# Performance work log

Measured on AMD Instinct MI355X. Metric: run time of the kernel, lower is better.

Reference implementation:

```python
import jax, jax.numpy as jnp
import numpy as np

HID = 128   # hidden_dim
NCLS = 10   # n_classes
B = 64      # number of graphs in the batched heterograph
NC, NP, NN = 100000, 400000, 150000  # component / port / net node counts
E = 400000  # edges per edge type


def setup_inputs() -> dict:
    key = jax.random.key(0)
    ks = jax.random.split(key, 32)
    f32 = jnp.float32

    def w(k, shape, fan_in):
        return jax.random.normal(k, shape, dtype=f32) * (1.0 / np.sqrt(fan_in))

    inp = {
        "h_comp": jax.random.normal(ks[0], (NC, 1), f32),
        "h_port": jax.random.normal(ks[1], (NP, 2), f32),
        "h_net": jax.random.normal(ks[2], (NN, 1), f32),
        "e_cp_src": jax.random.randint(ks[3], (E,), 0, NC, dtype=jnp.int32),
        "e_cp_dst": jax.random.randint(ks[4], (E,), 0, NP, dtype=jnp.int32),
        "e_pn_src": jax.random.randint(ks[5], (E,), 0, NP, dtype=jnp.int32),
        "e_pn_dst": jax.random.randint(ks[6], (E,), 0, NN, dtype=jnp.int32),
        "gid_comp": jnp.sort(jax.random.randint(ks[7], (NC,), 0, B, dtype=jnp.int32)),
        "gid_port": jnp.sort(jax.random.randint(ks[8], (NP,), 0, B, dtype=jnp.int32)),
        "gid_net": jnp.sort(jax.random.randint(ks[9], (NN,), 0, B, dtype=jnp.int32)),
        # GraphConv weights/biases per (layer, edge_type)
        "W1_cp": w(ks[10], (1, HID), 1), "b1_cp": jnp.zeros((HID,), f32),
        "W1_pn": w(ks[11], (2, HID), 2), "b1_pn": jnp.zeros((HID,), f32),
        "W2_cp": w(ks[12], (HID, HID), HID), "b2_cp": jnp.zeros((HID,), f32),
        "W2_pn": w(ks[13], (HID, HID), HID), "b2_pn": jnp.zeros((HID,), f32),
        "W3_cp": w(ks[14], (HID, HID), HID), "b3_cp": jnp.zeros((HID,), f32),
        "W3_pn": w(ks[15], (HID, HID), HID), "b3_pn": jnp.zeros((HID,), f32),
        # classify MLP (input dim 4 = 1+2+1 pooled original features)
        "Wc1": w(ks[16], (4, HID), 4), "bc1": jnp.zeros((HID,), f32),
        "Wc2": w(ks[17], (HID, HID), HID), "bc2": jnp.zeros((HID,), f32),
        "Wc3": w(ks[18], (HID, NCLS), HID), "bc3": jnp.zeros((NCLS,), f32),
    }
    return inp


def reference(h_comp, h_port, h_net,
              e_cp_src, e_cp_dst, e_pn_src, e_pn_dst,
              gid_comp, gid_port, gid_net,
              W1_cp, b1_cp, W1_pn, b1_pn,
              W2_cp, b2_cp, W2_pn, b2_pn,
              W3_cp, b3_cp, W3_pn, b3_pn,
              Wc1, bc1, Wc2, bc2, Wc3, bc3):
    seg = jax.ops.segment_sum

    # --- HeteroGraphConv layers (faithful to original forward, including its
    # bug: DGL HeteroGraphConv drops node types with no incoming relation, so
    # 'component' vanishes after conv1 and 'port' after conv2; conv3 runs on an
    # empty dict; conv outputs are never written back to g, hence dead code).
    # GraphConv(norm='none'): dst = sum_{edges} (x_src @ W) + b
    port1 = jax.nn.relu(seg((h_comp @ W1_cp)[e_cp_src], e_cp_dst, num_segments=NP) + b1_cp)
    net1 = jax.nn.relu(seg((h_port @ W1_pn)[e_pn_src], e_pn_dst, num_segments=NN) + b1_pn)
    net2 = jax.nn.relu(seg((port1 @ W2_pn)[e_pn_src], e_pn_dst, num_segments=NN) + b2_pn)
    # conv3: skipped entirely (no src types remain in the feature dict)
    del net1, net2  # never used by the original module's output path

    # --- dgl.mean_nodes reads g.nodes[*].data['h'] = ORIGINAL input features
    def gmean(x, gid):
        s = seg(x, gid, num_segments=B)
        c = seg(jnp.ones((x.shape[0], 1), x.dtype), gid, num_segments=B)
        return s / jnp.maximum(c, 1.0)

    hg = jnp.concatenate([gmean(h_comp, gid_comp),
                          gmean(h_port, gid_port),
                          gmean(h_net, gid_net)], axis=1)  # [B, 4]

    h = jax.nn.relu(hg @ Wc1 + bc1)
    h = jax.nn.relu(h @ Wc2 + bc2)
    return h @ Wc3 + bc3  # [B, n_classes]
```

## Files before the change

kernel.cpp:

```cpp
#include <hip/hip_runtime.h>
#include <hip/hip_bf16.h>


#define NGRAPH 64
#define NB_COMP 120
#define NB_PORT 723
#define NB_NET  181
#define NSLOT (NB_COMP + NB_PORT + NB_NET)


template <int NF>
__device__ void reduce_type(const float* __restrict__ h, const int* __restrict__ gid, int n,
                            float (*bins)[NGRAPH][4],
                            int nblocks, int bid) {
    int nv = (n + 3) >> 2;
    int per = (nv + nblocks - 1) / nblocks;
    int start = bid * per;
    int end = min(nv, start + per);
    int set = threadIdx.x & 3;

    int first = start * 4;
    int last = min(end * 4, n) - 1;
    if (first > last) return;

    int g_lo = gid[first];
    int g_hi = gid[last];

    if (g_lo == g_hi) {
        float s0 = 0.f, s1 = 0.f, cnt = 0.f;
        for (int iv = start + (int)threadIdx.x; iv < end; iv += (int)blockDim.x) {
            int i = iv * 4;
            if (i + 3 < n) {
                if (NF == 1) {
                    float4 hv = ((const float4*)h)[iv];
                    s0 += (hv.x + hv.y) + (hv.z + hv.w);
                } else {
                    float4 ha = ((const float4*)h)[iv * 2];
                    float4 hb = ((const float4*)h)[iv * 2 + 1];
                    s0 += ha.x + ha.z + hb.x + hb.z;
                    s1 += ha.y + ha.w + hb.y + hb.w;
                }
                cnt += 4.f;
            } else {
                for (int t = 0; t < 4 && i + t < n; ++t) {
                    if (NF == 1) { s0 += h[i + t]; }
                    else { s0 += h[(i + t) * 2]; s1 += h[(i + t) * 2 + 1]; }
                    cnt += 1.f;
                }
            }
        }
#pragma unroll
        for (int off = 32; off > 0; off >>= 1) {
            s0 += __shfl_down(s0, off);
            if (NF == 2) s1 += __shfl_down(s1, off);
            cnt += __shfl_down(cnt, off);
        }
        if ((threadIdx.x & 63) == 0) {
            int wset = threadIdx.x >> 6;
            atomicAdd(&bins[wset][g_lo][0], s0);
            if (NF == 2) atomicAdd(&bins[wset][g_lo][1], s1);
            atomicAdd(&bins[wset][g_lo][2], cnt);
        }
        return;
    }

    int cur = -1;
    float s0 = 0.f, s1 = 0.f, cnt = 0.f;

    for (int iv = start + (int)threadIdx.x; iv < end; iv += (int)blockDim.x) {
        int i = iv * 4;
        int g[4];
        float v0[4], v1[4];
        if (i + 3 < n) {
            int4 g4 = ((const int4*)gid)[iv];
            g[0] = g4.x; g[1] = g4.y; g[2] = g4.z; g[3] = g4.w;
            if (NF == 1) {
                float4 hv = ((const float4*)h)[iv];
                v0[0] = hv.x; v0[1] = hv.y; v0[2] = hv.z; v0[3] = hv.w;
            } else {
                float4 ha = ((const float4*)h)[iv * 2];
                float4 hb = ((const float4*)h)[iv * 2 + 1];
                v0[0] = ha.x; v1[0] = ha.y; v0[1] = ha.z; v1[1] = ha.w;
                v0[2] = hb.x; v1[2] = hb.y; v0[3] = hb.z; v1[3] = hb.w;
            }
        } else {
#pragma unroll
            for (int t = 0; t < 4; ++t) {
                if (i + t < n) {
                    g[t] = gid[i + t];
                    if (NF == 1) { v0[t] = h[i + t]; }
                    else { v0[t] = h[(i + t) * 2]; v1[t] = h[(i + t) * 2 + 1]; }
                } else {
                    g[t] = -2;
                    v0[t] = 0.f; v1[t] = 0.f;
                }
            }
        }
#pragma unroll
        for (int t = 0; t < 4; ++t) {
            if (g[t] == -2) continue;
            if (g[t] != cur) {
                if (cur >= 0) {
                    atomicAdd(&bins[set][cur][0], s0);
                    if (NF == 2) atomicAdd(&bins[set][cur][1], s1);
                    atomicAdd(&bins[set][cur][2], cnt);
                }
                cur = g[t]; s0 = 0.f; s1 = 0.f; cnt = 0.f;
            }
            s0 += v0[t];
            if (NF == 2) s1 += v1[t];
            cnt += 1.f;
        }
    }
    if (cur >= 0) {
        atomicAdd(&bins[set][cur][0], s0);
        if (NF == 2) atomicAdd(&bins[set][cur][1], s1);
        atomicAdd(&bins[set][cur][2], cnt);
    }
}

__global__ __launch_bounds__(256) void reduce_kernel(
    const float* __restrict__ h_comp, const float* __restrict__ h_port,
    const float* __restrict__ h_net,
    const int* __restrict__ gid_comp, const int* __restrict__ gid_port,
    const int* __restrict__ gid_net,
    int n_comp, int n_port, int n_net,
    float4* __restrict__ ws4) {
    __shared__ float bins[4][NGRAPH][4];
    int tid = threadIdx.x;
    int bid = blockIdx.x;

    for (int i = tid; i < 4 * NGRAPH * 4; i += 256) ((float*)bins)[i] = 0.f;
    __syncthreads();

    if (bid < NB_COMP) {
        reduce_type<1>(h_comp, gid_comp, n_comp, bins, NB_COMP, bid);
    } else if (bid < NB_COMP + NB_PORT) {
        reduce_type<2>(h_port, gid_port, n_port, bins, NB_PORT, bid - NB_COMP);
    } else {
        reduce_type<1>(h_net, gid_net, n_net, bins, NB_NET, bid - NB_COMP - NB_PORT);
    }
    __syncthreads();

    if (tid < NGRAPH) {
        float s0 = bins[0][tid][0] + bins[1][tid][0] + bins[2][tid][0] + bins[3][tid][0];
        float s1 = bins[0][tid][1] + bins[1][tid][1] + bins[2][tid][1] + bins[3][tid][1];
        float c  = bins[0][tid][2] + bins[1][tid][2] + bins[2][tid][2] + bins[3][tid][2];
        ws4[(size_t)tid * NSLOT + bid] = make_float4(s0, s1, c, 0.f);
    }
}

__global__ __launch_bounds__(256) void mlp_kernel(
    const float4* __restrict__ ws4,
    const float* __restrict__ Wc1, const float* __restrict__ bc1,
    const float* __restrict__ Wc2, const float* __restrict__ bc2,
    const float* __restrict__ Wc3, const float* __restrict__ bc3,
    float* __restrict__ out) {
    __shared__ float wred[4][8];
    __shared__ float hgs[4];
    __shared__ float h1[128];
    __shared__ float part[2][128];
    __shared__ float h2[128];
    __shared__ float l3[16][12];

    int g = blockIdx.x;
    int tid = threadIdx.x;

    float cs = 0.f, cc = 0.f, p0 = 0.f, p1 = 0.f, pc = 0.f, ns = 0.f, nc = 0.f;
    for (int s = tid; s < NSLOT; s += 256) {
        float4 v = ws4[(size_t)g * NSLOT + s];
        if (s < NB_COMP) { cs += v.x; cc += v.z; }
        else if (s < NB_COMP + NB_PORT) { p0 += v.x; p1 += v.y; pc += v.z; }
        else { ns += v.x; nc += v.z; }
    }
#pragma unroll
    for (int off = 32; off > 0; off >>= 1) {
        cs += __shfl_down(cs, off); cc += __shfl_down(cc, off);
        p0 += __shfl_down(p0, off); p1 += __shfl_down(p1, off);
        pc += __shfl_down(pc, off); ns += __shfl_down(ns, off);
        nc += __shfl_down(nc, off);
    }
    int wave = tid >> 6;
    if ((tid & 63) == 0) {
        wred[wave][0] = cs; wred[wave][1] = cc; wred[wave][2] = p0; wred[wave][3] = p1;
        wred[wave][4] = pc; wred[wave][5] = ns; wred[wave][6] = nc;
    }
    __syncthreads();
    if (tid == 0) {
        float t0 = wred[0][0] + wred[1][0] + wred[2][0] + wred[3][0];
        float t1 = wred[0][1] + wred[1][1] + wred[2][1] + wred[3][1];
        float t2 = wred[0][2] + wred[1][2] + wred[2][2] + wred[3][2];
        float t3 = wred[0][3] + wred[1][3] + wred[2][3] + wred[3][3];
        float t4 = wred[0][4] + wred[1][4] + wred[2][4] + wred[3][4];
        float t5 = wred[0][5] + wred[1][5] + wred[2][5] + wred[3][5];
        float t6 = wred[0][6] + wred[1][6] + wred[2][6] + wred[3][6];
        hgs[0] = t0 / fmaxf(t1, 1.f);
        hgs[1] = t2 / fmaxf(t4, 1.f);
        hgs[2] = t3 / fmaxf(t4, 1.f);
        hgs[3] = t5 / fmaxf(t6, 1.f);
    }
    __syncthreads();

    if (tid < 128) {
        float v = hgs[0] * Wc1[tid] + hgs[1] * Wc1[128 + tid] +
                  hgs[2] * Wc1[256 + tid] + hgs[3] * Wc1[384 + tid] + bc1[tid];
        h1[tid] = fmaxf(v, 0.f);
    }
    __syncthreads();

    {
        int j = tid & 127;
        int h = tid >> 7;
        float acc = 0.f;
#pragma unroll
        for (int kk = 0; kk < 64; kk += 4) {
            int k = h * 64 + kk;
            float4 hh = *(const float4*)&h1[k];
            acc += hh.x * Wc2[(k + 0) * 128 + j] + hh.y * Wc2[(k + 1) * 128 + j] +
                   hh.z * Wc2[(k + 2) * 128 + j] + hh.w * Wc2[(k + 3) * 128 + j];
        }
        part[h][j] = acc;
    }
    __syncthreads();
    if (tid < 128) h2[tid] = fmaxf(part[0][tid] + part[1][tid] + bc2[tid], 0.f);
    __syncthreads();

    if (tid < 160) {
        int c = tid % 10;
        int seg = tid / 10;
        float a = 0.f;
#pragma unroll
        for (int k = seg * 8; k < seg * 8 + 8; ++k) a += h2[k] * Wc3[k * 10 + c];
        l3[seg][c] = a;
    }
    __syncthreads();
    if (tid < 10) {
        float a = bc3[tid];
#pragma unroll
        for (int s = 0; s < 16; ++s) a += l3[s][tid];
        out[g * 10 + tid] = a;
    }
}

extern "C" void kernel_launch(void* const* d_in, const int* in_sizes, int n_in,
                              void* d_out, int out_size, void* d_ws, size_t ws_size,
                              hipStream_t stream) {
    const float* h_comp = (const float*)d_in[0];
    const float* h_port = (const float*)d_in[1];
    const float* h_net  = (const float*)d_in[2];
    const int* gid_comp = (const int*)d_in[7];
    const int* gid_port = (const int*)d_in[8];
    const int* gid_net  = (const int*)d_in[9];
    const float* Wc1 = (const float*)d_in[22];
    const float* bc1 = (const float*)d_in[23];
    const float* Wc2 = (const float*)d_in[24];
    const float* bc2 = (const float*)d_in[25];
    const float* Wc3 = (const float*)d_in[26];
    const float* bc3 = (const float*)d_in[27];

    int n_comp = in_sizes[0];
    int n_port = in_sizes[1] / 2;
    int n_net  = in_sizes[2];

    float4* ws4 = (float4*)d_ws;
    float* out = (float*)d_out;

    reduce_kernel<<<NSLOT, 256, 0, stream>>>(
        h_comp, h_port, h_net, gid_comp, gid_port, gid_net,
        n_comp, n_port, n_net, ws4);

    mlp_kernel<<<NGRAPH, 256, 0, stream>>>(ws4, Wc1, bc1, Wc2, bc2, Wc3, bc3, out);
}
```

Measured before the change: 119.3 us.

## Fuse segment-mean and MLP into one per-graph kernel using binary-searched ranges

Replaces the two-kernel design (1024-block atomic binning plus per-graph MLP) with a single kernel of 64 blocks, one per graph. Each block finds its contiguous node ranges in the sorted gid arrays through a wave-parallel 64-ary search, then sums the features directly with float4 loads and derives counts from the range lengths. This removes a kernel launch, the workspace round trip and the atomics. The cost is that only 64 blocks of 512 threads stream about 2.6 MB, which may underuse the GPU's memory bandwidth.

```diff
diff --git a/kernel.cpp b/kernel.cpp
--- a/kernel.cpp
+++ b/kernel.cpp
@@ -1,203 +1,132 @@
 #include <hip/hip_runtime.h>
-#include <hip/hip_bf16.h>
 
 
 #define NGRAPH 64
-#define NB_COMP 120
-#define NB_PORT 723
-#define NB_NET  181
-#define NSLOT (NB_COMP + NB_PORT + NB_NET)
-
-
-template <int NF>
-__device__ void reduce_type(const float* __restrict__ h, const int* __restrict__ gid, int n,
-                            float (*bins)[NGRAPH][4],
-                            int nblocks, int bid) {
-    int nv = (n + 3) >> 2;
-    int per = (nv + nblocks - 1) / nblocks;
-    int start = bid * per;
-    int end = min(nv, start + per);
-    int set = threadIdx.x & 3;
-
-    int first = start * 4;
-    int last = min(end * 4, n) - 1;
-    if (first > last) return;
-
-    int g_lo = gid[first];
-    int g_hi = gid[last];
-
-    if (g_lo == g_hi) {
-        float s0 = 0.f, s1 = 0.f, cnt = 0.f;
-        for (int iv = start + (int)threadIdx.x; iv < end; iv += (int)blockDim.x) {
-            int i = iv * 4;
-            if (i + 3 < n) {
-                if (NF == 1) {
-                    float4 hv = ((const float4*)h)[iv];
-                    s0 += (hv.x + hv.y) + (hv.z + hv.w);
-                } else {
-                    float4 ha = ((const float4*)h)[iv * 2];
-                    float4 hb = ((const float4*)h)[iv * 2 + 1];
-                    s0 += ha.x + ha.z + hb.x + hb.z;
-                    s1 += ha.y + ha.w + hb.y + hb.w;
-                }
-                cnt += 4.f;
-            } else {
-                for (int t = 0; t < 4 && i + t < n; ++t) {
-                    if (NF == 1) { s0 += h[i + t]; }
-                    else { s0 += h[(i + t) * 2]; s1 += h[(i + t) * 2 + 1]; }
-                    cnt += 1.f;
-                }
-            }
-        }
-#pragma unroll
-        for (int off = 32; off > 0; off >>= 1) {
-            s0 += __shfl_down(s0, off);
-            if (NF == 2) s1 += __shfl_down(s1, off);
-            cnt += __shfl_down(cnt, off);
-        }
-        if ((threadIdx.x & 63) == 0) {
-            int wset = threadIdx.x >> 6;
-            atomicAdd(&bins[wset][g_lo][0], s0);
-            if (NF == 2) atomicAdd(&bins[wset][g_lo][1], s1);
-            atomicAdd(&bins[wset][g_lo][2], cnt);
-        }
-        return;
-    }
-
-    int cur = -1;
-    float s0 = 0.f, s1 = 0.f, cnt = 0.f;
-
-    for (int iv = start + (int)threadIdx.x; iv < end; iv += (int)blockDim.x) {
-        int i = iv * 4;
-        int g[4];
-        float v0[4], v1[4];
-        if (i + 3 < n) {
-            int4 g4 = ((const int4*)gid)[iv];
-            g[0] = g4.x; g[1] = g4.y; g[2] = g4.z; g[3] = g4.w;
-            if (NF == 1) {
-                float4 hv = ((const float4*)h)[iv];
-                v0[0] = hv.x; v0[1] = hv.y; v0[2] = hv.z; v0[3] = hv.w;
-            } else {
-                float4 ha = ((const float4*)h)[iv * 2];
-                float4 hb = ((const float4*)h)[iv * 2 + 1];
-                v0[0] = ha.x; v1[0] = ha.y; v0[1] = ha.z; v1[1] = ha.w;
-                v0[2] = hb.x; v1[2] = hb.y; v0[3] = hb.z; v1[3] = hb.w;
-            }
+#define BLK 512
+
+__device__ __forceinline__ int wave_lb(const int* __restrict__ a, int n, int key) {
+    int lane = threadIdx.x & 63;
+    int lo = 0;
+    int len = n;
+    while (len > 0) {
+        int chunk = (len + 63) >> 6;
+        int off = lane * chunk;
+        bool valid = off < len;
+        int v = valid ? a[lo + off] : 0;
+        unsigned long long m = __ballot(valid && (v < key));
+        int c = __popcll(m);
+        if (c == 0) {
+            len = 0;
         } else {
-#pragma unroll
-            for (int t = 0; t < 4; ++t) {
-                if (i + t < n) {
-                    g[t] = gid[i + t];
-                    if (NF == 1) { v0[t] = h[i + t]; }
-                    else { v0[t] = h[(i + t) * 2]; v1[t] = h[(i + t) * 2 + 1]; }
-                } else {
-                    g[t] = -2;
-                    v0[t] = 0.f; v1[t] = 0.f;
-                }
-            }
-        }
-#pragma unroll
-        for (int t = 0; t < 4; ++t) {
-            if (g[t] == -2) continue;
-            if (g[t] != cur) {
-                if (cur >= 0) {
-                    atomicAdd(&bins[set][cur][0], s0);
-                    if (NF == 2) atomicAdd(&bins[set][cur][1], s1);
-                    atomicAdd(&bins[set][cur][2], cnt);
-                }
-                cur = g[t]; s0 = 0.f; s1 = 0.f; cnt = 0.f;
-            }
-            s0 += v0[t];
-            if (NF == 2) s1 += v1[t];
-            cnt += 1.f;
-        }
-    }
-    if (cur >= 0) {
-        atomicAdd(&bins[set][cur][0], s0);
-        if (NF == 2) atomicAdd(&bins[set][cur][1], s1);
-        atomicAdd(&bins[set][cur][2], cnt);
-    }
+            int nlo = lo + (c - 1) * chunk + 1;
+            int hi = lo + min(c * chunk, len);
+            lo = nlo;
+            len = hi - nlo;
+        }
+    }
+    return lo;
 }
 
-__global__ __launch_bounds__(256) void reduce_kernel(
+__global__ __launch_bounds__(BLK) void fused_kernel(
     const float* __restrict__ h_comp, const float* __restrict__ h_port,
     const float* __restrict__ h_net,
     const int* __restrict__ gid_comp, const int* __restrict__ gid_port,
     const int* __restrict__ gid_net,
     int n_comp, int n_port, int n_net,
-    float4* __restrict__ ws4) {
-    __shared__ float bins[4][NGRAPH][4];
-    int tid = threadIdx.x;
-    int bid = blockIdx.x;
-
-    for (int i = tid; i < 4 * NGRAPH * 4; i += 256) ((float*)bins)[i] = 0.f;
-    __syncthreads();
-
-    if (bid < NB_COMP) {
-        reduce_type<1>(h_comp, gid_comp, n_comp, bins, NB_COMP, bid);
-    } else if (bid < NB_COMP + NB_PORT) {
-        reduce_type<2>(h_port, gid_port, n_port, bins, NB_PORT, bid - NB_COMP);
-    } else {
-        reduce_type<1>(h_net, gid_net, n_net, bins, NB_NET, bid - NB_COMP - NB_PORT);
-    }
-    __syncthreads();
-
-    if (tid < NGRAPH) {
-        float s0 = bins[0][tid][0] + bins[1][tid][0] + bins[2][tid][0] + bins[3][tid][0];
-        float s1 = bins[0][tid][1] + bins[1][tid][1] + bins[2][tid][1] + bins[3][tid][1];
-        float c  = bins[0][tid][2] + bins[1][tid][2] + bins[2][tid][2] + bins[3][tid][2];
-        ws4[(size_t)tid * NSLOT + bid] = make_float4(s0, s1, c, 0.f);
-    }
-}
-
-__global__ __launch_bounds__(256) void mlp_kernel(
-    const float4* __restrict__ ws4,
     const float* __restrict__ Wc1, const float* __restrict__ bc1,
     const float* __restrict__ Wc2, const float* __restrict__ bc2,
     const float* __restrict__ Wc3, const float* __restrict__ bc3,
     float* __restrict__ out) {
-    __shared__ float wred[4][8];
+    __shared__ int rng[6];
+    __shared__ float wred[BLK / 64][4];
     __shared__ float hgs[4];
     __shared__ float h1[128];
-    __shared__ float part[2][128];
+    __shared__ float part[4][128];
     __shared__ float h2[128];
     __shared__ float l3[16][12];
 
-    int g = blockIdx.x;
-    int tid = threadIdx.x;
-
-    float cs = 0.f, cc = 0.f, p0 = 0.f, p1 = 0.f, pc = 0.f, ns = 0.f, nc = 0.f;
-    for (int s = tid; s < NSLOT; s += 256) {
-        float4 v = ws4[(size_t)g * NSLOT + s];
-        if (s < NB_COMP) { cs += v.x; cc += v.z; }
-        else if (s < NB_COMP + NB_PORT) { p0 += v.x; p1 += v.y; pc += v.z; }
-        else { ns += v.x; nc += v.z; }
-    }
+    const int g = blockIdx.x;
+    const int tid = threadIdx.x;
+    const int wave = tid >> 6;
+
+    if (wave == 0) {
+        int lo = wave_lb(gid_comp, n_comp, g);
+        int hi = wave_lb(gid_comp, n_comp, g + 1);
+        if ((tid & 63) == 0) { rng[0] = lo; rng[1] = hi; }
+    } else if (wave == 1) {
+        int lo = wave_lb(gid_port, n_port, g);
+        int hi = wave_lb(gid_port, n_port, g + 1);
+        if ((tid & 63) == 0) { rng[2] = lo; rng[3] = hi; }
+    } else if (wave == 2) {
+        int lo = wave_lb(gid_net, n_net, g);
+        int hi = wave_lb(gid_net, n_net, g + 1);
+        if ((tid & 63) == 0) { rng[4] = lo; rng[5] = hi; }
+    }
+    __syncthreads();
+
+    const int c0 = rng[0], c1 = rng[1];
+    const int p0 = rng[2], p1 = rng[3];
+    const int q0 = rng[4], q1 = rng[5];
+
+    float sc = 0.f, s0 = 0.f, s1 = 0.f, sn = 0.f;
+
+    {
+        int a4 = min(c1, (c0 + 3) & ~3);
+        for (int i = c0 + tid; i < a4; i += BLK) sc += h_comp[i];
+        int nv = (c1 - a4) >> 2;
+        const float4* hv = (const float4*)(h_comp + a4);
+        for (int iv = tid; iv < nv; iv += BLK) {
+            float4 v = hv[iv];
+            sc += (v.x + v.y) + (v.z + v.w);
+        }
+        for (int i = a4 + nv * 4 + tid; i < c1; i += BLK) sc += h_comp[i];
+    }
+    {
+        int a2 = min(p1, (p0 + 1) & ~1);
+        for (int i = p0 + tid; i < a2; i += BLK) { s0 += h_port[2 * i]; s1 += h_port[2 * i + 1]; }
+        int nv = (p1 - a2) >> 1;
+        const float4* hv = (const float4*)(h_port + 2 * a2);
+        for (int iv = tid; iv < nv; iv += BLK) {
+            float4 v = hv[iv];
+            s0 += v.x + v.z;
+            s1 += v.y + v.w;
+        }
+        for (int i = a2 + nv * 2 + tid; i < p1; i += BLK) { s0 += h_port[2 * i]; s1 += h_port[2 * i + 1]; }
+    }
+    {
+        int a4 = min(q1, (q0 + 3) & ~3);
+        for (int i = q0 + tid; i < a4; i += BLK) sn += h_net[i];
+        int nv = (q1 - a4) >> 2;
+        const float4* hv = (const float4*)(h_net + a4);
+        for (int iv = tid; iv < nv; iv += BLK) {
+            float4 v = hv[iv];
+            sn += (v.x + v.y) + (v.z + v.w);
+        }
+        for (int i = a4 + nv * 4 + tid; i < q1; i += BLK) sn += h_net[i];
+    }
+
 #pragma unroll
     for (int off = 32; off > 0; off >>= 1) {
-        cs += __shfl_down(cs, off); cc += __shfl_down(cc, off);
-        p0 += __shfl_down(p0, off); p1 += __shfl_down(p1, off);
-        pc += __shfl_down(pc, off); ns += __shfl_down(ns, off);
-        nc += __shfl_down(nc, off);
-    }
-    int wave = tid >> 6;
+        sc += __shfl_down(sc, off);
+        s0 += __shfl_down(s0, off);
+        s1 += __shfl_down(s1, off);
+        sn += __shfl_down(sn, off);
+    }
     if ((tid & 63) == 0) {
-        wred[wave][0] = cs; wred[wave][1] = cc; wred[wave][2] = p0; wred[wave][3] = p1;
-        wred[wave][4] = pc; wred[wave][5] = ns; wred[wave][6] = nc;
+        wred[wave][0] = sc; wred[wave][1] = s0;
+        wred[wave][2] = s1; wred[wave][3] = sn;
     }
     __syncthreads();
     if (tid == 0) {
-        float t0 = wred[0][0] + wred[1][0] + wred[2][0] + wred[3][0];
-        float t1 = wred[0][1] + wred[1][1] + wred[2][1] + wred[3][1];
-        float t2 = wred[0][2] + wred[1][2] + wred[2][2] + wred[3][2];
-        float t3 = wred[0][3] + wred[1][3] + wred[2][3] + wred[3][3];
-        float t4 = wred[0][4] + wred[1][4] + wred[2][4] + wred[3][4];
-        float t5 = wred[0][5] + wred[1][5] + wred[2][5] + wred[3][5];
-        float t6 = wred[0][6] + wred[1][6] + wred[2][6] + wred[3][6];
-        hgs[0] = t0 / fmaxf(t1, 1.f);
-        hgs[1] = t2 / fmaxf(t4, 1.f);
-        hgs[2] = t3 / fmaxf(t4, 1.f);
-        hgs[3] = t5 / fmaxf(t6, 1.f);
+        float a = 0.f, b = 0.f, c = 0.f, d = 0.f;
+#pragma unroll
+        for (int w = 0; w < BLK / 64; ++w) {
+            a += wred[w][0]; b += wred[w][1]; c += wred[w][2]; d += wred[w][3];
+        }
+        hgs[0] = a / fmaxf((float)(c1 - c0), 1.f);
+        hgs[1] = b / fmaxf((float)(p1 - p0), 1.f);
+        hgs[2] = c / fmaxf((float)(p1 - p0), 1.f);
+        hgs[3] = d / fmaxf((float)(q1 - q0), 1.f);
     }
     __syncthreads();
 
@@ -210,19 +139,20 @@
 
     {
         int j = tid & 127;
-        int h = tid >> 7;
+        int hq = tid >> 7;
         float acc = 0.f;
 #pragma unroll
-        for (int kk = 0; kk < 64; kk += 4) {
-            int k = h * 64 + kk;
+        for (int kk = 0; kk < 32; kk += 4) {
+            int k = hq * 32 + kk;
             float4 hh = *(const float4*)&h1[k];
             acc += hh.x * Wc2[(k + 0) * 128 + j] + hh.y * Wc2[(k + 1) * 128 + j] +
                    hh.z * Wc2[(k + 2) * 128 + j] + hh.w * Wc2[(k + 3) * 128 + j];
         }
-        part[h][j] = acc;
-    }
-    __syncthreads();
-    if (tid < 128) h2[tid] = fmaxf(part[0][tid] + part[1][tid] + bc2[tid], 0.f);
+        part[hq][j] = acc;
+    }
+    __syncthreads();
+    if (tid < 128)
+        h2[tid] = fmaxf(part[0][tid] + part[1][tid] + part[2][tid] + part[3][tid] + bc2[tid], 0.f);
     __syncthreads();
 
     if (tid < 160) {
@@ -262,12 +192,11 @@
     int n_port = in_sizes[1] / 2;
     int n_net  = in_sizes[2];
 
-    float4* ws4 = (float4*)d_ws;
     float* out = (float*)d_out;
-
-    reduce_kernel<<<NSLOT, 256, 0, stream>>>(
+    (void)d_ws; (void)ws_size;
+
+    fused_kernel<<<NGRAPH, BLK, 0, stream>>>(
         h_comp, h_port, h_net, gid_comp, gid_port, gid_net,
-        n_comp, n_port, n_net, ws4);
-
-    mlp_kernel<<<NGRAPH, 256, 0, stream>>>(ws4, Wc1, bc1, Wc2, bc2, Wc3, bc3, out);
+        n_comp, n_port, n_net,
+        Wc1, bc1, Wc2, bc2, Wc3, bc3, out);
 }
```

Result: faster. 116.6 us (-2.3%).
